# Performance work log

Hardware: AMD Instinct MI355X
Metric: run time of the kernel (lower is better)

Reference implementation:

```python
import jax, jax.numpy as jnp
import numpy as np

B, L, E, H, W = 2, 8192, 1024, 16, 128
HD = E // H  # 64


def setup_inputs() -> dict:
    key = jax.random.key(0)
    ks = jax.random.split(key, 9)
    s = 1.0 / np.sqrt(E)
    inp = {"x": jax.random.normal(ks[0], (B, L, E), jnp.float32)}
    for i, n in enumerate(["Wq", "Wk", "Wv", "Wo"]):
        inp[n] = jax.random.uniform(ks[1 + i], (E, E), jnp.float32, -s, s)
    for i, n in enumerate(["bq", "bk", "bv", "bo"]):
        inp[n] = jax.random.uniform(ks[5 + i], (E,), jnp.float32, -s, s)
    return inp


def _skew_prob(p, w):
    # (..., w, 2w+1) -> (..., w, 3w) with row i right-shifted by i:
    # out[..., i, i+j] = p[..., i, j]  (zeros elsewhere)
    lead = p.shape[:-2]
    M, Lc = p.shape[-2], p.shape[-1]
    p = jnp.pad(p, [(0, 0)] * len(lead) + [(0, 0), (0, M + 1)])
    p = p.reshape(*lead, M * (Lc + M + 1))[..., :-M].reshape(*lead, M, M + Lc)
    return p[..., :-1]


def _sliding_attend(q, k, v, w):
    # q,k,v: (b,h,l,d); banded attention, window w on each side (2w+1 diagonals)
    b, h, l, d = q.shape
    c = l // w
    qc = q.reshape(b, h, c, w, d)
    # per-chunk key/value windows of 3w tokens (w halo each side, zero padded)
    idx = jnp.arange(c)[:, None] * w + jnp.arange(3 * w)[None, :]  # (c, 3w)
    kw = jnp.pad(k, ((0, 0), (0, 0), (w, w), (0, 0)))[:, :, idx]  # (b,h,c,3w,d)
    s = jnp.einsum('bhcqd,bhckd->bhcqk', qc, kw)  # (b,h,c,w,3w)
    # extract band: band[i, j] = s[i, i+j], j in [0, 2w] (offset d = j - w)
    gidx = (jnp.arange(w)[:, None] + jnp.arange(2 * w + 1)[None, :])[None, None, None]
    band = jnp.take_along_axis(s, gidx, axis=-1).reshape(b, h, l, 2 * w + 1)
    # mask out-of-range positions (matches the module's edge -inf loop)
    pos = jnp.arange(l)[:, None] + (jnp.arange(2 * w + 1) - w)[None, :]
    band = jnp.where((pos >= 0) & (pos < l), band, -jnp.inf)
    prob = jax.nn.softmax(band / np.sqrt(d), axis=-1)  # scale by sqrt(head_dim)
    vw = jnp.pad(v, ((0, 0), (0, 0), (w, w), (0, 0)))[:, :, idx]  # (b,h,c,3w,d)
    p3 = _skew_prob(prob.reshape(b, h, c, w, 2 * w + 1), w)  # (b,h,c,w,3w)
    ctx = jnp.einsum('bhcqk,bhckd->bhcqd', p3, vw)
    return ctx.reshape(b, h, l, d)


def reference(x, Wq, Wk, Wv, Wo, bq, bk, bv, bo):
    q = (x @ Wq.T + bq).reshape(B, L, H, HD).transpose(0, 2, 1, 3)
    k = (x @ Wk.T + bk).reshape(B, L, H, HD).transpose(0, 2, 1, 3)
    v = (x @ Wv.T + bv).reshape(B, L, H, HD).transpose(0, 2, 1, 3)
    ctx = _sliding_attend(q, k, v, W)
    ctx = ctx.transpose(0, 2, 1, 3).reshape(B, L, E)
    return ctx @ Wo.T + bo
```

## Files before the change

kernel.cpp:

```cpp
#include <hip/hip_runtime.h>
#include <math.h>

#define B_SZ  2
#define L_SEQ 8192
#define EMB   1024
#define NH    16
#define HDIM  64
#define WIN   128
#define MROWS (B_SZ*L_SEQ)

typedef __attribute__((ext_vector_type(8))) _Float16 f16x8;
typedef __attribute__((ext_vector_type(4))) _Float16 f16x4;
typedef __attribute__((ext_vector_type(4))) float f32x4;

__device__ __forceinline__ void gload16(const void* g, void* l) {
    __builtin_amdgcn_global_load_lds(
        (const __attribute__((address_space(1))) unsigned int*)g,
        (__attribute__((address_space(3))) unsigned int*)l, 16, 0, 0);
}

__global__ __launch_bounds__(256)
void round_all(const float* __restrict__ x,
               const float* __restrict__ wq, const float* __restrict__ wk,
               const float* __restrict__ wv, const float* __restrict__ wo,
               _Float16* __restrict__ xf, _Float16* __restrict__ q16,
               _Float16* __restrict__ k16, _Float16* __restrict__ v16,
               _Float16* __restrict__ o16)
{
    const size_t NX = (size_t)MROWS * EMB, NW = (size_t)EMB * EMB;
    size_t gid = ((size_t)blockIdx.x * 256 + threadIdx.x) * 4;
    const float* src; _Float16* dst; size_t off;
    if (gid < NX)               { src = x;  dst = xf;  off = gid; }
    else if (gid < NX + NW)     { src = wq; dst = q16; off = gid - NX; }
    else if (gid < NX + 2*NW)   { src = wk; dst = k16; off = gid - NX - 2*NW + NW; }
    else if (gid < NX + 3*NW)   { src = wv; dst = v16; off = gid - NX - 2*NW; }
    else                        { src = wo; dst = o16; off = gid - NX - 3*NW; }
    float4 v = *(const float4*)(src + off);
    f16x4 o;
    o[0] = (_Float16)v.x; o[1] = (_Float16)v.y;
    o[2] = (_Float16)v.z; o[3] = (_Float16)v.w;
    *(f16x4*)(dst + off) = o;
}


#define STAGE_HT(ptr_, tb_, op_, h_, kt_)                                      \
    {                                                                          \
        char* d_ = smem + (op_) * 65536 + ((kt_) & 1) * 32768 + (h_) * 16384 + ldst; \
        const _Float16* s_ = (ptr_) + ((size_t)((tb_) + (h_) * 128 + srow6)) * 1024 + (kt_) * 64 + gch; \
        gload16(s_, d_);                                                       \
        gload16(s_ + 64 * 1024, d_ + 8192);                                    \
    }

#define DSREAD_A(qr_)                                                          \
    _Pragma("unroll")                                                          \
    for (int i_ = 0; i_ < 4; ++i_) {                                           \
        const int ro_ = (qr_) * 8192 + (i_ * 16 + frow) * 128;                 \
        af[i_][0] = *(const f16x8*)(Ab + ro_ + sb0);                           \
        af[i_][1] = *(const f16x8*)(Ab + ro_ + sb1);                           \
    }

#define DSREAD_B(qc_)                                                          \
    _Pragma("unroll")                                                          \
    for (int j_ = 0; j_ < 2; ++j_) {                                           \
        const int ro_ = (brow + (qc_) * 32 + j_ * 16 + frow) * 128;            \
        bf[j_][0] = *(const f16x8*)(Bb + ro_ + sb0);                           \
        bf[j_][1] = *(const f16x8*)(Bb + ro_ + sb1);                           \
    }

#define MFMA16(qr_, qc_)                                                       \
    __builtin_amdgcn_s_setprio(1);                                             \
    _Pragma("unroll")                                                          \
    for (int ks_ = 0; ks_ < 2; ++ks_)                                          \
        _Pragma("unroll")                                                      \
        for (int i_ = 0; i_ < 4; ++i_)                                         \
            _Pragma("unroll")                                                  \
            for (int j_ = 0; j_ < 2; ++j_)                                     \
                acc[(qr_) * 4 + i_][(qc_) * 2 + j_] =                          \
                    __builtin_amdgcn_mfma_f32_16x16x32_f16(                    \
                        af[i_][ks_], bf[j_][ks_],                              \
                        acc[(qr_) * 4 + i_][(qc_) * 2 + j_], 0, 0, 0);         \
    __builtin_amdgcn_s_setprio(0);

#define BARM()                                                                 \
    asm volatile("" ::: "memory");                                             \
    __builtin_amdgcn_s_barrier();                                              \
    asm volatile("" ::: "memory");

#define GEMM8_CORE(Aptr, Bptr)                                                 \
    const int t = threadIdx.x;                                                 \
    const int wave = t >> 6, lane = t & 63;                                    \
    const int wr = wave >> 2, wc = wave & 3;                                   \
    const int frow = lane & 15, quad = lane >> 4;                              \
    const int srow6 = t >> 3;                                                  \
    const int gch = ((t & 7) ^ (srow6 & 7)) * 8;                               \
    const int ldst = t * 16;                                                   \
    const int sb0 = (quad ^ (frow & 7)) * 16, sb1 = sb0 ^ 64;                  \
    const int brow = (wc & 1) * 64;                                            \
    f32x4 acc[8][4] = {};                                                      \
    f16x8 af[4][2], bf[2][2];                                                  \
    STAGE_HT(Aptr, bm, 0, 0, 0) STAGE_HT(Aptr, bm, 0, 1, 0)                    \
    STAGE_HT(Bptr, bn, 1, 0, 0) STAGE_HT(Bptr, bn, 1, 1, 0)                    \
    for (int kt = 0; kt < 16; ++kt) {                                          \
        const char* Ab = smem + (kt & 1) * 32768 + wr * 16384;                 \
        const char* Bb = smem + 65536 + (kt & 1) * 32768 + (wc >> 1) * 16384;  \
        if (kt < 15) {                                                         \
            STAGE_HT(Aptr, bm, 0, 0, kt + 1)                                   \
            asm volatile("s_waitcnt vmcnt(2)" ::: "memory");                   \
        } else {                                                               \
            asm volatile("s_waitcnt vmcnt(0)" ::: "memory");                   \
        }                                                                      \
        BARM()                                                                 \
        DSREAD_A(0) DSREAD_B(0)                  \
        MFMA16(0, 0)                                                           \
        DSREAD_B(1)                            \
        if (kt < 15) STAGE_HT(Aptr, bm, 0, 1, kt + 1)                          \
        BARM()                                                                 \
        MFMA16(0, 1)                                                           \
        DSREAD_A(1)                                                            \
        if (kt < 15) STAGE_HT(Bptr, bn, 1, 0, kt + 1)                          \
        BARM()                                                                 \
        MFMA16(1, 1)                                                           \
        DSREAD_B(0)                                \
        if (kt < 15) STAGE_HT(Bptr, bn, 1, 1, kt + 1)                          \
        BARM()                                                                 \
        MFMA16(1, 0)                                                           \
        BARM()                                                                 \
    }

__global__ __launch_bounds__(512, 2)
void gemm_qkv(const _Float16* __restrict__ X,
              const _Float16* __restrict__ Wq, const _Float16* __restrict__ Wk,
              const _Float16* __restrict__ Wv,
              const float* __restrict__ bq, const float* __restrict__ bk,
              const float* __restrict__ bv,
              _Float16* __restrict__ qf, _Float16* __restrict__ kf,
              _Float16* __restrict__ vtf)
{
    __shared__ __attribute__((aligned(16))) char smem[131072];

    const int id = blockIdx.x;
    const int row = (id / 96) * 8 + (id & 7);
    const int colq = (id >> 3) % 12;
    const int wsel = colq >> 2;
    const int bm = row * 256, bn = (colq & 3) * 256;
    const _Float16* Bw = wsel == 0 ? Wq : wsel == 1 ? Wk : Wv;
    const float* bias = wsel == 0 ? bq : wsel == 1 ? bk : bv;
    const float scale = wsel == 0 ? 0.125f : 1.0f;

    GEMM8_CORE(X, Bw)

    char* Cw = smem + wave * 8192;
    const int bb = bm >> 13;
    const int l0 = (bm & (L_SEQ - 1)) + wr * 128;
    const int h = (bn >> 6) + wc;
    if (wsel < 2) {
        _Float16* dst = wsel == 0 ? qf : kf;
        const size_t hb = ((size_t)(bb * NH + h)) * L_SEQ * HDIM;
        #pragma unroll
        for (int ih = 0; ih < 2; ++ih) {
            asm volatile("" ::: "memory");
            #pragma unroll
            for (int i = 0; i < 4; ++i)
                #pragma unroll
                for (int j = 0; j < 4; ++j) {
                    const int lc = j * 16 + frow;
                    const float bvv = bias[bn + wc * 64 + lc];
                    #pragma unroll
                    for (int r = 0; r < 4; ++r) {
                        const int lr = i * 16 + quad * 4 + r;
                        const int bo = lr * 128 + ((lc * 2) ^ ((lr & 7) << 4));
                        *(_Float16*)(Cw + bo) = (_Float16)((acc[ih * 4 + i][j][r] + bvv) * scale);
                    }
                }
            asm volatile("" ::: "memory");
            #pragma unroll
            for (int p = 0; p < 8; ++p) {
                const int idx = p * 64 + lane;
                const int lr = idx >> 3, seg = idx & 7;
                const int bo = lr * 128 + ((seg * 16) ^ ((lr & 7) << 4));
                uint4 v = *(const uint4*)(Cw + bo);
                *(uint4*)&dst[hb + (size_t)(l0 + ih * 64 + lr) * HDIM + seg * 8] = v;
            }
        }
    } else {
        const size_t hb = ((size_t)(bb * NH + h)) * HDIM * L_SEQ;
        #pragma unroll
        for (int ih = 0; ih < 2; ++ih) {
            asm volatile("" ::: "memory");
            #pragma unroll
            for (int i = 0; i < 4; ++i)
                #pragma unroll
                for (int j = 0; j < 4; ++j) {
                    const int lc = j * 16 + frow;
                    const float bvv = bias[bn + wc * 64 + lc];
                    #pragma unroll
                    for (int r = 0; r < 4; ++r) {
                        const int lr = i * 16 + quad * 4 + r;
                        const int bo = lc * 128 + ((lr * 2) ^ ((lc & 7) << 4));
                        *(_Float16*)(Cw + bo) = (_Float16)(acc[ih * 4 + i][j][r] + bvv);
                    }
                }
            asm volatile("" ::: "memory");
            #pragma unroll
            for (int p = 0; p < 8; ++p) {
                const int idx = p * 64 + lane;
                const int dc = idx >> 3, sl = idx & 7;
                const int bo = dc * 128 + ((sl * 16) ^ ((dc & 7) << 4));
                uint4 v = *(const uint4*)(Cw + bo);
                *(uint4*)&vtf[hb + (size_t)dc * L_SEQ + (l0 + ih * 64 + sl * 8)] = v;
            }
        }
    }
}

__global__ __launch_bounds__(512, 2)
void gemm_out(const _Float16* __restrict__ A, const _Float16* __restrict__ Bwm,
              const float* __restrict__ bias, float* __restrict__ C)
{
    constexpr int N = EMB;
    __shared__ __attribute__((aligned(16))) char smem[131072];

    const int id = blockIdx.x;
    const int row = (id / 32) * 8 + (id & 7);
    const int bm = row * 256, bn = ((id >> 3) & 3) * 256;

    GEMM8_CORE(A, Bwm)

    #pragma unroll
    for (int i = 0; i < 8; ++i) {
        int m0 = bm + wr * 128 + i * 16 + quad * 4;
        #pragma unroll
        for (int j = 0; j < 4; ++j) {
            int n = bn + wc * 64 + j * 16 + frow;
            float bvv = bias[n];
            #pragma unroll
            for (int r = 0; r < 4; ++r)
                C[(size_t)(m0 + r) * N + n] = acc[i][j][r] + bvv;
        }
    }
}

__global__ __launch_bounds__(256)
void attn_mfma(const _Float16* __restrict__ qf, const _Float16* __restrict__ kf,
               const _Float16* __restrict__ vtf, _Float16* __restrict__ cf)
{
    __shared__ _Float16 Kf[2][4096], Vf[2][4096];
    __shared__ _Float16 Ps[4][16 * 72];

    const int t = threadIdx.x;
    const int wave = t >> 6, lane = t & 63;
    const int col = lane & 15, quad = lane >> 4;
    const int bh = blockIdx.y;
    const int q0 = blockIdx.x * 128;

    f16x8 qfr[2][2];
    #pragma unroll
    for (int g = 0; g < 2; g++) {
        size_t qidx = ((size_t)bh * L_SEQ + q0 + g * 64 + wave * 16 + col) * HDIM + quad * 8;
        qfr[g][0] = *(const f16x8*)(qf + qidx);
        qfr[g][1] = *(const f16x8*)(qf + qidx + 32);
    }

    f32x4 o[2][4] = {};
    float lsum[2][4] = {};

    const int srow = t >> 3, sc = t & 7;
    _Float16* Pw = Ps[wave];

    const int ktlo = (q0 == 0) ? 2 : 0;
    const int kthi = (q0 == L_SEQ - 128) ? 4 : 6;

#define STAGE_KV(kt_, bsel_)                                                   \
    {                                                                          \
        const int p0s = q0 - WIN + (kt_) * 64;                                 \
        _Pragma("unroll")                                                      \
        for (int sw2 = 0; sw2 < 2; sw2++) {                                    \
            int rowk = sw2 * 32 + srow;                                        \
            int gq = sc ^ (rowk & 7);                                          \
            size_t kgi = ((size_t)bh * L_SEQ + p0s + rowk) * HDIM + gq * 8;    \
            size_t vgi = ((size_t)bh * HDIM + rowk) * L_SEQ + p0s + gq * 8;    \
            int lb = sw2 * 4096 + wave * 1024;                                 \
            gload16(kf + kgi, (char*)&Kf[bsel_][0] + lb);                      \
            gload16(vtf + vgi, (char*)&Vf[bsel_][0] + lb);                     \
        }                                                                      \
    }

    STAGE_KV(ktlo, 0)

    for (int kt = ktlo; kt < kthi; kt++) {
        const int p0 = q0 - WIN + kt * 64;
        const int rel = kt * 64 - WIN;
        const int cb = (kt - ktlo) & 1;
        if (kt + 1 < kthi) {
            STAGE_KV(kt + 1, cb ^ 1)
            asm volatile("s_waitcnt vmcnt(4)" ::: "memory");
        } else {
            asm volatile("s_waitcnt vmcnt(0)" ::: "memory");
        }
        __builtin_amdgcn_s_barrier();
        asm volatile("" ::: "memory");

        const char* Kb = (const char*)&Kf[cb][0];
        const char* Vb = (const char*)&Vf[cb][0];

        #pragma unroll
        for (int g = 0; g < 2; g++) {
            const int oo = g * 64 + wave * 16;
            if (rel < oo - 191 || rel > oo + 143) continue;
            f32x4 s[4] = {};
            #pragma unroll
            for (int ks = 0; ks < 2; ks++)
                #pragma unroll
                for (int n = 0; n < 4; n++) {
                    int off = (n * 16 + col) * 128 + (((ks * 4 + quad) ^ (col & 7)) * 16);
                    f16x8 kfr = *(const f16x8*)(Kb + off);
                    s[n] = __builtin_amdgcn_mfma_f32_16x16x32_f16(qfr[g][ks], kfr, s[n], 0, 0, 0);
                }
            const int rowb = q0 + oo + quad * 4;
            #pragma unroll
            for (int n = 0; n < 4; n++)
                #pragma unroll
                for (int r = 0; r < 4; r++) {
                    int dlt = (p0 + n * 16 + col) - (rowb + r);
                    if (dlt < -WIN || dlt > WIN) s[n][r] = -3e38f;
                }
            #pragma unroll
            for (int n = 0; n < 4; n++)
                #pragma unroll
                for (int r = 0; r < 4; r++) {
                    float pv = __expf(s[n][r]);
                    lsum[g][r] += pv;
                    Pw[(quad * 4 + r) * 72 + n * 16 + col] = (_Float16)pv;
                }
            #pragma unroll
            for (int ks = 0; ks < 2; ks++) {
                f16x8 pfr = *(const f16x8*)&Pw[col * 72 + ks * 32 + quad * 8];
                #pragma unroll
                for (int n = 0; n < 4; n++) {
                    int off = (n * 16 + col) * 128 + (((ks * 4 + quad) ^ (col & 7)) * 16);
                    f16x8 vfr = *(const f16x8*)(Vb + off);
                    o[g][n] = __builtin_amdgcn_mfma_f32_16x16x32_f16(pfr, vfr, o[g][n], 0, 0, 0);
                }
            }
        }
        asm volatile("" ::: "memory");
        __builtin_amdgcn_s_barrier();
        asm volatile("" ::: "memory");
    }

    #pragma unroll
    for (int g = 0; g < 2; g++)
        #pragma unroll
        for (int x = 1; x < 16; x <<= 1)
            #pragma unroll
            for (int r = 0; r < 4; r++)
                lsum[g][r] += __shfl_xor(lsum[g][r], x, 64);

    const int b = bh >> 4, h = bh & 15;
    #pragma unroll
    for (int g = 0; g < 2; g++)
        #pragma unroll
        for (int r = 0; r < 4; r++) {
            float inv = 1.0f / lsum[g][r];
            int q = q0 + g * 64 + wave * 16 + quad * 4 + r;
            size_t base = ((size_t)b * L_SEQ + q) * EMB + h * HDIM;
            #pragma unroll
            for (int n = 0; n < 4; n++)
                cf[base + n * 16 + col] = (_Float16)(o[g][n][r] * inv);
        }
}

extern "C" void kernel_launch(void* const* d_in, const int* in_sizes, int n_in,
                              void* d_out, int out_size, void* d_ws, size_t ws_size,
                              hipStream_t stream) {
    const float* x  = (const float*)d_in[0];
    const float* Wq = (const float*)d_in[1];
    const float* Wk = (const float*)d_in[2];
    const float* Wv = (const float*)d_in[3];
    const float* Wo = (const float*)d_in[4];
    const float* bq = (const float*)d_in[5];
    const float* bk = (const float*)d_in[6];
    const float* bv = (const float*)d_in[7];
    const float* bo = (const float*)d_in[8];
    float* out = (float*)d_out;

    const size_t per = (size_t)B_SZ * NH * L_SEQ * HDIM;
    _Float16* w16 = (_Float16*)d_ws;
    _Float16* xf   = w16;
    _Float16* qf   = w16 + per;
    _Float16* kf   = w16 + 2 * per;
    _Float16* vtf  = w16 + 3 * per;
    _Float16* cf   = w16 + 4 * per;
    _Float16* wq16 = w16 + 5 * per;
    _Float16* wk16 = wq16 + 1048576;
    _Float16* wv16 = wq16 + 2 * 1048576;
    _Float16* wo16 = wq16 + 3 * 1048576;

    const int nround = (MROWS * EMB + 4 * EMB * EMB) / 1024;
    round_all<<<nround, dim3(256), 0, stream>>>(x, Wq, Wk, Wv, Wo, xf, wq16, wk16, wv16, wo16);

    gemm_qkv<<<768, dim3(512), 0, stream>>>(xf, wq16, wk16, wv16, bq, bk, bv, qf, kf, vtf);

    attn_mfma<<<dim3(L_SEQ / 128, B_SZ * NH), dim3(256), 0, stream>>>(qf, kf, vtf, cf);

    gemm_out<<<256, dim3(512), 0, stream>>>(cf, wo16, bo, out);
}
```

Measured before the change: 333.3 us.

## Use 8 waves per attention block, one 16-row query tile each

The attention kernel moves from 256 to 512 threads, so each of 8 waves owns one 16-row query tile where before 4 waves each processed two. K/V staging is spread across all 512 threads with one load each, and the wait count is adjusted to match. The band mask is now applied only to tiles that touch the window edges. This raises parallelism per block and lowers register pressure per wave, at the cost of more threads sharing each barrier.

```diff
diff --git a/kernel.cpp b/kernel.cpp
--- a/kernel.cpp
+++ b/kernel.cpp
@@ -240,29 +240,29 @@
     }
 }
 
-__global__ __launch_bounds__(256)
+__global__ __launch_bounds__(512)
 void attn_mfma(const _Float16* __restrict__ qf, const _Float16* __restrict__ kf,
                const _Float16* __restrict__ vtf, _Float16* __restrict__ cf)
 {
     __shared__ _Float16 Kf[2][4096], Vf[2][4096];
-    __shared__ _Float16 Ps[4][16 * 72];
+    __shared__ _Float16 Ps[8][16 * 72];
 
     const int t = threadIdx.x;
     const int wave = t >> 6, lane = t & 63;
     const int col = lane & 15, quad = lane >> 4;
     const int bh = blockIdx.y;
     const int q0 = blockIdx.x * 128;
-
-    f16x8 qfr[2][2];
-    #pragma unroll
-    for (int g = 0; g < 2; g++) {
-        size_t qidx = ((size_t)bh * L_SEQ + q0 + g * 64 + wave * 16 + col) * HDIM + quad * 8;
-        qfr[g][0] = *(const f16x8*)(qf + qidx);
-        qfr[g][1] = *(const f16x8*)(qf + qidx + 32);
-    }
-
-    f32x4 o[2][4] = {};
-    float lsum[2][4] = {};
+    const int oo = wave * 16;
+
+    f16x8 qfr[2];
+    {
+        size_t qidx = ((size_t)bh * L_SEQ + q0 + oo + col) * HDIM + quad * 8;
+        qfr[0] = *(const f16x8*)(qf + qidx);
+        qfr[1] = *(const f16x8*)(qf + qidx + 32);
+    }
+
+    f32x4 o[4] = {};
+    float lsum[4] = {};
 
     const int srow = t >> 3, sc = t & 7;
     _Float16* Pw = Ps[wave];
@@ -273,27 +273,21 @@
 #define STAGE_KV(kt_, bsel_)                                                   \
     {                                                                          \
         const int p0s = q0 - WIN + (kt_) * 64;                                 \
-        _Pragma("unroll")                                                      \
-        for (int sw2 = 0; sw2 < 2; sw2++) {                                    \
-            int rowk = sw2 * 32 + srow;                                        \
-            int gq = sc ^ (rowk & 7);                                          \
-            size_t kgi = ((size_t)bh * L_SEQ + p0s + rowk) * HDIM + gq * 8;    \
-            size_t vgi = ((size_t)bh * HDIM + rowk) * L_SEQ + p0s + gq * 8;    \
-            int lb = sw2 * 4096 + wave * 1024;                                 \
-            gload16(kf + kgi, (char*)&Kf[bsel_][0] + lb);                      \
-            gload16(vtf + vgi, (char*)&Vf[bsel_][0] + lb);                     \
-        }                                                                      \
+        const int gq = sc ^ (srow & 7);                                        \
+        size_t kgi = ((size_t)bh * L_SEQ + p0s + srow) * HDIM + gq * 8;        \
+        size_t vgi = ((size_t)bh * HDIM + srow) * L_SEQ + p0s + gq * 8;        \
+        gload16(kf + kgi, (char*)&Kf[bsel_][0] + t * 16);                      \
+        gload16(vtf + vgi, (char*)&Vf[bsel_][0] + t * 16);                     \
     }
 
     STAGE_KV(ktlo, 0)
 
     for (int kt = ktlo; kt < kthi; kt++) {
         const int p0 = q0 - WIN + kt * 64;
-        const int rel = kt * 64 - WIN;
         const int cb = (kt - ktlo) & 1;
         if (kt + 1 < kthi) {
             STAGE_KV(kt + 1, cb ^ 1)
-            asm volatile("s_waitcnt vmcnt(4)" ::: "memory");
+            asm volatile("s_waitcnt vmcnt(2)" ::: "memory");
         } else {
             asm volatile("s_waitcnt vmcnt(0)" ::: "memory");
         }
@@ -303,10 +297,8 @@
         const char* Kb = (const char*)&Kf[cb][0];
         const char* Vb = (const char*)&Vf[cb][0];
 
-        #pragma unroll
-        for (int g = 0; g < 2; g++) {
-            const int oo = g * 64 + wave * 16;
-            if (rel < oo - 191 || rel > oo + 143) continue;
+        const int relp = kt * 64 - WIN - oo;
+        if (relp >= -191 && relp <= 143) {
             f32x4 s[4] = {};
             #pragma unroll
             for (int ks = 0; ks < 2; ks++)
@@ -314,22 +306,24 @@
                 for (int n = 0; n < 4; n++) {
                     int off = (n * 16 + col) * 128 + (((ks * 4 + quad) ^ (col & 7)) * 16);
                     f16x8 kfr = *(const f16x8*)(Kb + off);
-                    s[n] = __builtin_amdgcn_mfma_f32_16x16x32_f16(qfr[g][ks], kfr, s[n], 0, 0, 0);
-                }
-            const int rowb = q0 + oo + quad * 4;
-            #pragma unroll
-            for (int n = 0; n < 4; n++)
-                #pragma unroll
-                for (int r = 0; r < 4; r++) {
-                    int dlt = (p0 + n * 16 + col) - (rowb + r);
-                    if (dlt < -WIN || dlt > WIN) s[n][r] = -3e38f;
-                }
+                    s[n] = __builtin_amdgcn_mfma_f32_16x16x32_f16(qfr[ks], kfr, s[n], 0, 0, 0);
+                }
+            if (relp < -113 || relp > 65) {
+                const int rowb = q0 + oo + quad * 4;
+                #pragma unroll
+                for (int n = 0; n < 4; n++)
+                    #pragma unroll
+                    for (int r = 0; r < 4; r++) {
+                        int dlt = (p0 + n * 16 + col) - (rowb + r);
+                        if (dlt < -WIN || dlt > WIN) s[n][r] = -3e38f;
+                    }
+            }
             #pragma unroll
             for (int n = 0; n < 4; n++)
                 #pragma unroll
                 for (int r = 0; r < 4; r++) {
                     float pv = __expf(s[n][r]);
-                    lsum[g][r] += pv;
+                    lsum[r] += pv;
                     Pw[(quad * 4 + r) * 72 + n * 16 + col] = (_Float16)pv;
                 }
             #pragma unroll
@@ -339,7 +333,7 @@
                 for (int n = 0; n < 4; n++) {
                     int off = (n * 16 + col) * 128 + (((ks * 4 + quad) ^ (col & 7)) * 16);
                     f16x8 vfr = *(const f16x8*)(Vb + off);
-                    o[g][n] = __builtin_amdgcn_mfma_f32_16x16x32_f16(pfr, vfr, o[g][n], 0, 0, 0);
+                    o[n] = __builtin_amdgcn_mfma_f32_16x16x32_f16(pfr, vfr, o[n], 0, 0, 0);
                 }
             }
         }
@@ -349,25 +343,21 @@
     }
 
     #pragma unroll
-    for (int g = 0; g < 2; g++)
-        #pragma unroll
-        for (int x = 1; x < 16; x <<= 1)
-            #pragma unroll
-            for (int r = 0; r < 4; r++)
-                lsum[g][r] += __shfl_xor(lsum[g][r], x, 64);
+    for (int x = 1; x < 16; x <<= 1)
+        #pragma unroll
+        for (int r = 0; r < 4; r++)
+            lsum[r] += __shfl_xor(lsum[r], x, 64);
 
     const int b = bh >> 4, h = bh & 15;
     #pragma unroll
-    for (int g = 0; g < 2; g++)
-        #pragma unroll
-        for (int r = 0; r < 4; r++) {
-            float inv = 1.0f / lsum[g][r];
-            int q = q0 + g * 64 + wave * 16 + quad * 4 + r;
-            size_t base = ((size_t)b * L_SEQ + q) * EMB + h * HDIM;
-            #pragma unroll
-            for (int n = 0; n < 4; n++)
-                cf[base + n * 16 + col] = (_Float16)(o[g][n][r] * inv);
-        }
+    for (int r = 0; r < 4; r++) {
+        float inv = 1.0f / lsum[r];
+        int q = q0 + oo + quad * 4 + r;
+        size_t base = ((size_t)b * L_SEQ + q) * EMB + h * HDIM;
+        #pragma unroll
+        for (int n = 0; n < 4; n++)
+            cf[base + n * 16 + col] = (_Float16)(o[n][r] * inv);
+    }
 }
 
 extern "C" void kernel_launch(void* const* d_in, const int* in_sizes, int n_in,
@@ -401,7 +391,7 @@
 
     gemm_qkv<<<768, dim3(512), 0, stream>>>(xf, wq16, wk16, wv16, bq, bk, bv, qf, kf, vtf);
 
-    attn_mfma<<<dim3(L_SEQ / 128, B_SZ * NH), dim3(256), 0, stream>>>(qf, kf, vtf, cf);
+    attn_mfma<<<dim3(L_SEQ / 128, B_SZ * NH), dim3(512), 0, stream>>>(qf, kf, vtf, cf);
 
     gemm_out<<<256, dim3(512), 0, stream>>>(cf, wo16, bo, out);
 }
```

Measured after the change: 325.6 us. 1.02x faster.
